# Optimization experiments

Measured on AMD Instinct MI355X. Metric: run time of the kernel, lower is better.

The kernel has to match this reference:

```python
import jax, jax.numpy as jnp
import numpy as np

B, S, D, H = 2, 2048, 1024, 16  # batch, seq, embed_dim, num_heads
DH = D // H                      # head dim = 64


def setup_inputs() -> dict:
    key = jax.random.key(0)
    kx, kq, kbq, kk, kbk, kv, kbv = jax.random.split(key, 7)
    scale = 1.0 / np.sqrt(D)
    return {
        "x": jax.random.normal(kx, (B, S, D), dtype=jnp.float32),
        "Wq": jax.random.normal(kq, (D, D), dtype=jnp.float32) * scale,
        "bq": jax.random.normal(kbq, (D,), dtype=jnp.float32) * 0.01,
        "Wk": jax.random.normal(kk, (D, D), dtype=jnp.float32) * scale,
        "bk": jax.random.normal(kbk, (D,), dtype=jnp.float32) * 0.01,
        "Wv": jax.random.normal(kv, (D, D), dtype=jnp.float32) * scale,
        "bv": jax.random.normal(kbv, (D,), dtype=jnp.float32) * 0.01,
    }


def reference(x, Wq, bq, Wk, bk, Wv, bv):
    # ooqkv_type == 'q', odeint_method == 'id': q branch = act(Linear(x)), exact GELU (torch nn.GELU default)
    q = jax.nn.gelu(x @ Wq + bq, approximate=False)
    k = x @ Wk + bk
    v = x @ Wv + bv
    # [B, S, D] -> [B, S, H, DH]
    q = q.reshape(B, S, H, DH)
    k = k.reshape(B, S, H, DH)
    v = v.reshape(B, S, H, DH)
    # NOTE: original module has NO 1/sqrt(d) scale — faithful reproduction
    att = jnp.einsum("bqhd,bkhd->bhqk", q, k)
    att = jax.nn.softmax(att, axis=-1)
    out = jnp.einsum("bhqk,bkhd->bqhd", att, v)
    return out.reshape(B, S, D)
```

## Files before the change

kernel.cpp:

```cpp
#include <hip/hip_runtime.h>
#include <math.h>

#define B_  2
#define S_  2048
#define D_  1024
#define H_  16
#define DH_ 64
#define M_  (B_ * S_)

typedef _Float16 half_t;
typedef __attribute__((ext_vector_type(8))) _Float16 h8;
typedef __attribute__((ext_vector_type(4))) _Float16 h4;
typedef __attribute__((ext_vector_type(4))) float   f32x4;

#define LOG2E 1.44269504088896f

__device__ __forceinline__ void gll16(const half_t* g, half_t* l) {
    __builtin_amdgcn_global_load_lds(
        (__attribute__((address_space(1))) const void*)g,
        (__attribute__((address_space(3))) void*)l, 16, 0, 0);
}

__global__ __launch_bounds__(256) void convert_x_k(
    const float* __restrict__ x, half_t* __restrict__ xh)
{
    const size_t i = ((size_t)blockIdx.x * 256 + threadIdx.x) * 8;
    const float4 a = *(const float4*)(x + i);
    const float4 b = *(const float4*)(x + i + 4);
    h8 o;
    o[0] = (half_t)a.x; o[1] = (half_t)a.y; o[2] = (half_t)a.z; o[3] = (half_t)a.w;
    o[4] = (half_t)b.x; o[5] = (half_t)b.y; o[6] = (half_t)b.z; o[7] = (half_t)b.w;
    *(h8*)(xh + i) = o;
}

__global__ __launch_bounds__(256) void transW_k(
    const float* __restrict__ Wq, const float* __restrict__ Wk,
    const float* __restrict__ Wv, half_t* __restrict__ Wt)
{
    const int which = blockIdx.y;
    const float* __restrict__ W = (which == 0) ? Wq : (which == 1) ? Wk : Wv;
    half_t* __restrict__ T = Wt + (size_t)which * D_ * D_;
    const int gw   = blockIdx.x * 4 + (threadIdx.x >> 6);
    const int lane = threadIdx.x & 63;
    const int n    = (gw & 15) * 64 + lane;
    const int k0   = (gw >> 4) * 8;
    h8 o;
    #pragma unroll
    for (int t = 0; t < 8; ++t) o[t] = (half_t)W[(size_t)(k0 + t) * D_ + n];
    *(h8*)(T + (size_t)n * D_ + k0) = o;
}

__global__ __launch_bounds__(256) void transV_k(
    const half_t* __restrict__ V, half_t* __restrict__ Vt)
{
    const int gw   = blockIdx.x * 4 + (threadIdx.x >> 6);
    const int lane = threadIdx.x & 63;
    const int bh   = gw >> 8;
    const int s0   = (gw & 255) * 8;
    const int b    = bh >> 4, h = bh & 15;
    h8 o;
    #pragma unroll
    for (int t = 0; t < 8; ++t)
        o[t] = V[((size_t)b * S_ + s0 + t) * D_ + h * DH_ + lane];
    *(h8*)(Vt + ((size_t)bh * DH_ + lane) * S_ + s0) = o;
}

__global__ __launch_bounds__(256) void qkv_gemm_f16(
    const half_t* __restrict__ xh, const half_t* __restrict__ Wt,
    const float* __restrict__ bq, const float* __restrict__ bk,
    const float* __restrict__ bv,
    half_t* __restrict__ Qo, half_t* __restrict__ Ko, half_t* __restrict__ Vo)
{
    const int n0g   = blockIdx.x * 128;
    const int which = n0g >> 10;
    const int n0    = n0g & 1023;
    const int m0    = blockIdx.y * 128;
    const half_t* __restrict__ Wp  = Wt + (size_t)which * D_ * D_;
    const float* __restrict__ bias = (which == 0) ? bq : (which == 1) ? bk : bv;
    half_t* __restrict__ out       = (which == 0) ? Qo : (which == 1) ? Ko : Vo;

    const int tid = threadIdx.x, lane = tid & 63, wave = tid >> 6;
    const int wm = (wave >> 1) * 64, wn = (wave & 1) * 64;
    const int ln = lane & 15, quad = lane >> 4;

    __shared__ __align__(16) half_t As[128][32];
    __shared__ __align__(16) half_t Bs[128][32];

    f32x4 acc[4][4];
    #pragma unroll
    for (int i = 0; i < 4; ++i)
        #pragma unroll
        for (int j = 0; j < 4; ++j) acc[i][j] = (f32x4){0.f, 0.f, 0.f, 0.f};

    for (int k0 = 0; k0 < D_; k0 += 32) {
        __syncthreads();
        #pragma unroll
        for (int l = 0; l < 2; ++l) {
            const int c = tid + l * 256;
            const int r = c >> 2, c8 = c & 3;
            gll16(xh + (size_t)(m0 + r) * D_ + k0 + c8 * 8, &As[r][c8 * 8]);
            gll16(Wp + (size_t)(n0 + r) * D_ + k0 + c8 * 8, &Bs[r][c8 * 8]);
        }
        __syncthreads();

        h8 af[4], bf[4];
        #pragma unroll
        for (int i = 0; i < 4; ++i) af[i] = *(const h8*)&As[wm + i * 16 + ln][quad * 8];
        #pragma unroll
        for (int j = 0; j < 4; ++j) bf[j] = *(const h8*)&Bs[wn + j * 16 + ln][quad * 8];
        #pragma unroll
        for (int i = 0; i < 4; ++i)
            #pragma unroll
            for (int j = 0; j < 4; ++j)
                acc[i][j] = __builtin_amdgcn_mfma_f32_16x16x32_f16(
                    af[i], bf[j], acc[i][j], 0, 0, 0);
    }

    #pragma unroll
    for (int j = 0; j < 4; ++j) {
        const int col = n0 + wn + j * 16 + ln;
        const float bb = bias[col];
        #pragma unroll
        for (int i = 0; i < 4; ++i) {
            #pragma unroll
            for (int r = 0; r < 4; ++r) {
                const int row = m0 + wm + i * 16 + quad * 4 + r;
                float t = acc[i][j][r] + bb;
                if (which == 0) {
                    const float u = t * fmaf(t * t, 0.0356774081f, 0.7978845608f);
                    const float e = __builtin_amdgcn_exp2f(u * -2.88539008178f);
                    t = t * __builtin_amdgcn_rcpf(1.0f + e) * LOG2E;
                }
                out[(size_t)row * D_ + col] = (half_t)t;
            }
        }
    }
}

__global__ __launch_bounds__(256) void attn_f16(
    const half_t* __restrict__ Q, const half_t* __restrict__ K,
    const half_t* __restrict__ Vt, float* __restrict__ out)
{
    const int tid  = threadIdx.x;
    const int lane = tid & 63;
    const int wave = tid >> 6;
    const int ln   = lane & 15;
    const int quad = lane >> 4;
    const int bh   = blockIdx.y;
    const int b    = bh >> 4;
    const int h    = bh & 15;
    const int q0   = blockIdx.x * 64;

    const half_t* __restrict__ Qb  = Q  + (size_t)b * S_ * D_ + h * DH_;
    const half_t* __restrict__ Kb  = K  + (size_t)b * S_ * D_ + h * DH_;
    const half_t* __restrict__ Vtb = Vt + (size_t)bh * DH_ * S_;

    __shared__ __align__(16) half_t Ks[64 * 64];
    __shared__ __align__(16) half_t Vs[64 * 64];
    __shared__ __align__(16) half_t QPs[64][72];

    #pragma unroll
    for (int l = 0; l < 2; ++l) {
        const int c = tid + l * 256;
        const int r = c >> 3, k8 = c & 7;
        *(h8*)&QPs[r][k8 * 8] = *(const h8*)(Qb + (size_t)(q0 + r) * D_ + k8 * 8);
    }
    __syncthreads();
    const h8 qb0 = *(const h8*)&QPs[wave * 16 + ln][quad * 8];
    const h8 qb1 = *(const h8*)&QPs[wave * 16 + ln][32 + quad * 8];

    h8 ones8;
    #pragma unroll
    for (int t = 0; t < 8; ++t) ones8[t] = (half_t)1.0f;

    f32x4 O[4];
    #pragma unroll
    for (int j = 0; j < 4; ++j) O[j] = (f32x4){0.f, 0.f, 0.f, 0.f};
    f32x4 l5 = (f32x4){0.f, 0.f, 0.f, 0.f};
    float m_i = -INFINITY;

    for (int k0 = 0; k0 < S_; k0 += 64) {
        __syncthreads();
        #pragma unroll
        for (int l = 0; l < 2; ++l) {
            const int c = tid + l * 256;
            const int r = c >> 3, c0 = c & 7;
            const int cs = c0 ^ (r & 7);
            gll16(Kb  + (size_t)(k0 + r) * D_ + cs * 8, &Ks[c * 8]);
            gll16(Vtb + (size_t)r * S_ + k0 + cs * 8,   &Vs[c * 8]);
        }
        __syncthreads();

        f32x4 s[4];
        #pragma unroll
        for (int j = 0; j < 4; ++j) {
            const int rK = j * 16 + ln;
            const h8 ka0 = *(const h8*)&Ks[rK * 64 + ((quad)     ^ (rK & 7)) * 8];
            const h8 ka1 = *(const h8*)&Ks[rK * 64 + ((quad + 4) ^ (rK & 7)) * 8];
            f32x4 t = (f32x4){0.f, 0.f, 0.f, 0.f};
            t = __builtin_amdgcn_mfma_f32_16x16x32_f16(ka0, qb0, t, 0, 0, 0);
            t = __builtin_amdgcn_mfma_f32_16x16x32_f16(ka1, qb1, t, 0, 0, 0);
            s[j] = t;
        }

        float mx = fmaxf(fmaxf(fmaxf(s[0][0], s[0][1]), fmaxf(s[0][2], s[0][3])),
                         fmaxf(fmaxf(s[1][0], s[1][1]), fmaxf(s[1][2], s[1][3])));
        mx = fmaxf(mx, fmaxf(fmaxf(fmaxf(s[2][0], s[2][1]), fmaxf(s[2][2], s[2][3])),
                             fmaxf(fmaxf(s[3][0], s[3][1]), fmaxf(s[3][2], s[3][3]))));
        mx = fmaxf(mx, __shfl_xor(mx, 16, 64));
        mx = fmaxf(mx, __shfl_xor(mx, 32, 64));

        if (__ballot(mx > m_i)) {
            const float mnew  = fmaxf(m_i, mx);
            const float alpha = __builtin_amdgcn_exp2f(m_i - mnew);
            m_i = mnew;
            float ar[4];
            #pragma unroll
            for (int r = 0; r < 4; ++r) ar[r] = __shfl(alpha, quad * 4 + r, 64);
            #pragma unroll
            for (int r = 0; r < 4; ++r) {
                l5[r] *= ar[r];
                #pragma unroll
                for (int j = 0; j < 4; ++j) O[j][r] *= ar[r];
            }
        }

        #pragma unroll
        for (int j = 0; j < 4; ++j) {
            h4 pv;
            #pragma unroll
            for (int r = 0; r < 4; ++r)
                pv[r] = (half_t)__builtin_amdgcn_exp2f(s[j][r] - m_i);
            *(h4*)&QPs[wave * 16 + ln][j * 16 + quad * 4] = pv;
        }

        const h8 pa0 = *(const h8*)&QPs[wave * 16 + ln][quad * 8];
        const h8 pa1 = *(const h8*)&QPs[wave * 16 + ln][32 + quad * 8];
        #pragma unroll
        for (int j = 0; j < 4; ++j) {
            const int rV = j * 16 + ln;
            const h8 vb0 = *(const h8*)&Vs[rV * 64 + ((quad)     ^ (rV & 7)) * 8];
            const h8 vb1 = *(const h8*)&Vs[rV * 64 + ((quad + 4) ^ (rV & 7)) * 8];
            O[j] = __builtin_amdgcn_mfma_f32_16x16x32_f16(pa0, vb0, O[j], 0, 0, 0);
            O[j] = __builtin_amdgcn_mfma_f32_16x16x32_f16(pa1, vb1, O[j], 0, 0, 0);
        }
        l5 = __builtin_amdgcn_mfma_f32_16x16x32_f16(pa0, ones8, l5, 0, 0, 0);
        l5 = __builtin_amdgcn_mfma_f32_16x16x32_f16(pa1, ones8, l5, 0, 0, 0);
    }

    #pragma unroll
    for (int r = 0; r < 4; ++r) {
        const float inv = 1.0f / l5[r];
        const int row = q0 + wave * 16 + quad * 4 + r;
        #pragma unroll
        for (int j = 0; j < 4; ++j)
            out[((size_t)b * S_ + row) * D_ + h * DH_ + j * 16 + ln] = O[j][r] * inv;
    }
}

extern "C" void kernel_launch(void* const* d_in, const int* in_sizes, int n_in,
                              void* d_out, int out_size, void* d_ws, size_t ws_size,
                              hipStream_t stream) {
    const float* x  = (const float*)d_in[0];
    const float* Wq = (const float*)d_in[1];
    const float* bq = (const float*)d_in[2];
    const float* Wk = (const float*)d_in[3];
    const float* bk = (const float*)d_in[4];
    const float* Wv = (const float*)d_in[5];
    const float* bv = (const float*)d_in[6];
    float* out = (float*)d_out;

    const size_t nmd = (size_t)M_ * D_;
    const size_t ndd = (size_t)D_ * D_;
    half_t* xh  = (half_t*)d_ws;
    half_t* Wt  = xh + nmd;
    half_t* Qh  = Wt + 3 * ndd;
    half_t* Kh  = Qh + nmd;
    half_t* Vh  = Kh + nmd;
    half_t* Vtw = Vh + nmd;

    convert_x_k<<<nmd / (256 * 8), 256, 0, stream>>>(x, xh);
    transW_k<<<dim3(512, 3), 256, 0, stream>>>(Wq, Wk, Wv, Wt);
    qkv_gemm_f16<<<dim3(3 * D_ / 128, M_ / 128), 256, 0, stream>>>(
        xh, Wt, bq, bk, bv, Qh, Kh, Vh);
    transV_k<<<2048, 256, 0, stream>>>(Vh, Vtw);
    attn_f16<<<dim3(S_ / 64, B_ * H_), 256, 0, stream>>>(Qh, Kh, Vtw, out);
}
```

Before: 197.9 us.

## Fuse prep kernels, write V transposed from GEMM, widen GEMM K-tile and attention Q-tile

```diff
diff --git a/kernel.cpp b/kernel.cpp
--- a/kernel.cpp
+++ b/kernel.cpp
@@ -21,55 +21,41 @@
         (__attribute__((address_space(3))) void*)l, 16, 0, 0);
 }
 
-__global__ __launch_bounds__(256) void convert_x_k(
-    const float* __restrict__ x, half_t* __restrict__ xh)
-{
-    const size_t i = ((size_t)blockIdx.x * 256 + threadIdx.x) * 8;
-    const float4 a = *(const float4*)(x + i);
-    const float4 b = *(const float4*)(x + i + 4);
-    h8 o;
-    o[0] = (half_t)a.x; o[1] = (half_t)a.y; o[2] = (half_t)a.z; o[3] = (half_t)a.w;
-    o[4] = (half_t)b.x; o[5] = (half_t)b.y; o[6] = (half_t)b.z; o[7] = (half_t)b.w;
-    *(h8*)(xh + i) = o;
-}
-
-__global__ __launch_bounds__(256) void transW_k(
+__global__ __launch_bounds__(256) void prep_k(
+    const float* __restrict__ x, half_t* __restrict__ xh,
     const float* __restrict__ Wq, const float* __restrict__ Wk,
     const float* __restrict__ Wv, half_t* __restrict__ Wt)
 {
-    const int which = blockIdx.y;
-    const float* __restrict__ W = (which == 0) ? Wq : (which == 1) ? Wk : Wv;
-    half_t* __restrict__ T = Wt + (size_t)which * D_ * D_;
-    const int gw   = blockIdx.x * 4 + (threadIdx.x >> 6);
-    const int lane = threadIdx.x & 63;
-    const int n    = (gw & 15) * 64 + lane;
-    const int k0   = (gw >> 4) * 8;
-    h8 o;
-    #pragma unroll
-    for (int t = 0; t < 8; ++t) o[t] = (half_t)W[(size_t)(k0 + t) * D_ + n];
-    *(h8*)(T + (size_t)n * D_ + k0) = o;
-}
-
-__global__ __launch_bounds__(256) void transV_k(
-    const half_t* __restrict__ V, half_t* __restrict__ Vt)
-{
-    const int gw   = blockIdx.x * 4 + (threadIdx.x >> 6);
-    const int lane = threadIdx.x & 63;
-    const int bh   = gw >> 8;
-    const int s0   = (gw & 255) * 8;
-    const int b    = bh >> 4, h = bh & 15;
-    h8 o;
-    #pragma unroll
-    for (int t = 0; t < 8; ++t)
-        o[t] = V[((size_t)b * S_ + s0 + t) * D_ + h * DH_ + lane];
-    *(h8*)(Vt + ((size_t)bh * DH_ + lane) * S_ + s0) = o;
+    const int bx = blockIdx.x;
+    if (bx < 2048) {
+        const size_t i = ((size_t)bx * 256 + threadIdx.x) * 8;
+        const float4 a = *(const float4*)(x + i);
+        const float4 b = *(const float4*)(x + i + 4);
+        h8 o;
+        o[0] = (half_t)a.x; o[1] = (half_t)a.y; o[2] = (half_t)a.z; o[3] = (half_t)a.w;
+        o[4] = (half_t)b.x; o[5] = (half_t)b.y; o[6] = (half_t)b.z; o[7] = (half_t)b.w;
+        *(h8*)(xh + i) = o;
+    } else {
+        const int gb    = bx - 2048;
+        const int which = gb >> 9;
+        const float* __restrict__ W = (which == 0) ? Wq : (which == 1) ? Wk : Wv;
+        half_t* __restrict__ T = Wt + (size_t)which * D_ * D_;
+        const int gw   = (gb & 511) * 4 + (threadIdx.x >> 6);
+        const int lane = threadIdx.x & 63;
+        const int n    = (gw & 15) * 64 + lane;
+        const int k0   = (gw >> 4) * 8;
+        h8 o;
+        #pragma unroll
+        for (int t = 0; t < 8; ++t) o[t] = (half_t)W[(size_t)(k0 + t) * D_ + n];
+        *(h8*)(T + (size_t)n * D_ + k0) = o;
+    }
 }
 
 __global__ __launch_bounds__(256) void qkv_gemm_f16(
     const half_t* __restrict__ xh, const half_t* __restrict__ Wt,
     const float* __restrict__ bq, const float* __restrict__ bk,
     const float* __restrict__ bv,
-    half_t* __restrict__ Qo, half_t* __restrict__ Ko, half_t* __restrict__ Vo)
+    half_t* __restrict__ Qo, half_t* __restrict__ Ko, half_t* __restrict__ Vt)
 {
     const int n0g   = blockIdx.x * 128;
     const int which = n0g >> 10;
@@ -77,14 +63,13 @@
     const int m0    = blockIdx.y * 128;
     const half_t* __restrict__ Wp  = Wt + (size_t)which * D_ * D_;
     const float* __restrict__ bias = (which == 0) ? bq : (which == 1) ? bk : bv;
-    half_t* __restrict__ out       = (which == 0) ? Qo : (which == 1) ? Ko : Vo;
 
     const int tid = threadIdx.x, lane = tid & 63, wave = tid >> 6;
     const int wm = (wave >> 1) * 64, wn = (wave & 1) * 64;
     const int ln = lane & 15, quad = lane >> 4;
 
-    __shared__ __align__(16) half_t As[128][32];
-    __shared__ __align__(16) half_t Bs[128][32];
+    __shared__ __align__(16) half_t As[128 * 64];
+    __shared__ __align__(16) half_t Bs[128 * 64];
 
     f32x4 acc[4][4];
     #pragma unroll
@@ -92,46 +77,75 @@
         #pragma unroll
         for (int j = 0; j < 4; ++j) acc[i][j] = (f32x4){0.f, 0.f, 0.f, 0.f};
 
-    for (int k0 = 0; k0 < D_; k0 += 32) {
+    for (int k0 = 0; k0 < D_; k0 += 64) {
         __syncthreads();
         #pragma unroll
-        for (int l = 0; l < 2; ++l) {
-            const int c = tid + l * 256;
-            const int r = c >> 2, c8 = c & 3;
-            gll16(xh + (size_t)(m0 + r) * D_ + k0 + c8 * 8, &As[r][c8 * 8]);
-            gll16(Wp + (size_t)(n0 + r) * D_ + k0 + c8 * 8, &Bs[r][c8 * 8]);
+        for (int l = 0; l < 4; ++l) {
+            const int c  = tid + l * 256;
+            const int r  = c >> 3, c0 = c & 7;
+            const int cs = c0 ^ (r & 7);
+            gll16(xh + (size_t)(m0 + r) * D_ + k0 + cs * 8, &As[c * 8]);
+            gll16(Wp + (size_t)(n0 + r) * D_ + k0 + cs * 8, &Bs[c * 8]);
         }
         __syncthreads();
 
-        h8 af[4], bf[4];
-        #pragma unroll
-        for (int i = 0; i < 4; ++i) af[i] = *(const h8*)&As[wm + i * 16 + ln][quad * 8];
-        #pragma unroll
-        for (int j = 0; j < 4; ++j) bf[j] = *(const h8*)&Bs[wn + j * 16 + ln][quad * 8];
-        #pragma unroll
-        for (int i = 0; i < 4; ++i)
-            #pragma unroll
-            for (int j = 0; j < 4; ++j)
-                acc[i][j] = __builtin_amdgcn_mfma_f32_16x16x32_f16(
-                    af[i], bf[j], acc[i][j], 0, 0, 0);
-    }
-
-    #pragma unroll
-    for (int j = 0; j < 4; ++j) {
-        const int col = n0 + wn + j * 16 + ln;
-        const float bb = bias[col];
-        #pragma unroll
-        for (int i = 0; i < 4; ++i) {
-            #pragma unroll
-            for (int r = 0; r < 4; ++r) {
-                const int row = m0 + wm + i * 16 + quad * 4 + r;
-                float t = acc[i][j][r] + bb;
-                if (which == 0) {
-                    const float u = t * fmaf(t * t, 0.0356774081f, 0.7978845608f);
-                    const float e = __builtin_amdgcn_exp2f(u * -2.88539008178f);
-                    t = t * __builtin_amdgcn_rcpf(1.0f + e) * LOG2E;
+        #pragma unroll
+        for (int kc = 0; kc < 2; ++kc) {
+            h8 af[4], bf[4];
+            #pragma unroll
+            for (int i = 0; i < 4; ++i) {
+                const int r = wm + i * 16 + ln;
+                af[i] = *(const h8*)&As[r * 64 + (((kc << 2) + quad) ^ (r & 7)) * 8];
+            }
+            #pragma unroll
+            for (int j = 0; j < 4; ++j) {
+                const int r = wn + j * 16 + ln;
+                bf[j] = *(const h8*)&Bs[r * 64 + (((kc << 2) + quad) ^ (r & 7)) * 8];
+            }
+            #pragma unroll
+            for (int i = 0; i < 4; ++i)
+                #pragma unroll
+                for (int j = 0; j < 4; ++j)
+                    acc[i][j] = __builtin_amdgcn_mfma_f32_16x16x32_f16(
+                        af[i], bf[j], acc[i][j], 0, 0, 0);
+        }
+    }
+
+    if (which == 2) {
+        #pragma unroll
+        for (int j = 0; j < 4; ++j) {
+            const int col = n0 + wn + j * 16 + ln;
+            const int h = col >> 6, d = col & 63;
+            const float bb = bias[col];
+            #pragma unroll
+            for (int i = 0; i < 4; ++i) {
+                const int sg = m0 + wm + i * 16 + quad * 4;
+                const int b  = sg >> 11, srow = sg & 2047;
+                h4 pv;
+                #pragma unroll
+                for (int r = 0; r < 4; ++r) pv[r] = (half_t)(acc[i][j][r] + bb);
+                *(h4*)(Vt + (((size_t)(b * H_ + h) * DH_ + d) * S_ + srow)) = pv;
+            }
+        }
+    } else {
+        half_t* __restrict__ out = (which == 0) ? Qo : Ko;
+        #pragma unroll
+        for (int j = 0; j < 4; ++j) {
+            const int col = n0 + wn + j * 16 + ln;
+            const float bb = bias[col];
+            #pragma unroll
+            for (int i = 0; i < 4; ++i) {
+                #pragma unroll
+                for (int r = 0; r < 4; ++r) {
+                    const int row = m0 + wm + i * 16 + quad * 4 + r;
+                    float t = acc[i][j][r] + bb;
+                    if (which == 0) {
+                        const float u = t * fmaf(t * t, 0.0356774081f, 0.7978845608f);
+                        const float e = __builtin_amdgcn_exp2f(u * -2.88539008178f);
+                        t = t * __builtin_amdgcn_rcpf(1.0f + e) * LOG2E;
+                    }
+                    out[(size_t)row * D_ + col] = (half_t)t;
                 }
-                out[(size_t)row * D_ + col] = (half_t)t;
             }
         }
     }
@@ -149,7 +163,7 @@
     const int bh   = blockIdx.y;
     const int b    = bh >> 4;
     const int h    = bh & 15;
-    const int q0   = blockIdx.x * 64;
+    const int q0   = blockIdx.x * 128;
 
     const half_t* __restrict__ Qb  = Q  + (size_t)b * S_ * D_ + h * DH_;
     const half_t* __restrict__ Kb  = K  + (size_t)b * S_ * D_ + h * DH_;
@@ -157,104 +171,138 @@
 
     __shared__ __align__(16) half_t Ks[64 * 64];
     __shared__ __align__(16) half_t Vs[64 * 64];
-    __shared__ __align__(16) half_t QPs[64][72];
-
-    #pragma unroll
-    for (int l = 0; l < 2; ++l) {
+    __shared__ __align__(16) half_t QPs[128][72];
+
+    #pragma unroll
+    for (int l = 0; l < 4; ++l) {
         const int c = tid + l * 256;
         const int r = c >> 3, k8 = c & 7;
         *(h8*)&QPs[r][k8 * 8] = *(const h8*)(Qb + (size_t)(q0 + r) * D_ + k8 * 8);
     }
     __syncthreads();
-    const h8 qb0 = *(const h8*)&QPs[wave * 16 + ln][quad * 8];
-    const h8 qb1 = *(const h8*)&QPs[wave * 16 + ln][32 + quad * 8];
+    const h8 qa0 = *(const h8*)&QPs[wave * 32 + ln][quad * 8];
+    const h8 qa1 = *(const h8*)&QPs[wave * 32 + ln][32 + quad * 8];
+    const h8 qc0 = *(const h8*)&QPs[wave * 32 + 16 + ln][quad * 8];
+    const h8 qc1 = *(const h8*)&QPs[wave * 32 + 16 + ln][32 + quad * 8];
 
     h8 ones8;
     #pragma unroll
     for (int t = 0; t < 8; ++t) ones8[t] = (half_t)1.0f;
 
-    f32x4 O[4];
-    #pragma unroll
-    for (int j = 0; j < 4; ++j) O[j] = (f32x4){0.f, 0.f, 0.f, 0.f};
-    f32x4 l5 = (f32x4){0.f, 0.f, 0.f, 0.f};
-    float m_i = -INFINITY;
+    f32x4 Oa[4], Ob[4];
+    #pragma unroll
+    for (int j = 0; j < 4; ++j) {
+        Oa[j] = (f32x4){0.f, 0.f, 0.f, 0.f};
+        Ob[j] = (f32x4){0.f, 0.f, 0.f, 0.f};
+    }
+    f32x4 la = (f32x4){0.f, 0.f, 0.f, 0.f};
+    f32x4 lb = (f32x4){0.f, 0.f, 0.f, 0.f};
+    float m_a = -INFINITY, m_b = -INFINITY;
 
     for (int k0 = 0; k0 < S_; k0 += 64) {
         __syncthreads();
         #pragma unroll
         for (int l = 0; l < 2; ++l) {
-            const int c = tid + l * 256;
-            const int r = c >> 3, c0 = c & 7;
+            const int c  = tid + l * 256;
+            const int r  = c >> 3, c0 = c & 7;
             const int cs = c0 ^ (r & 7);
             gll16(Kb  + (size_t)(k0 + r) * D_ + cs * 8, &Ks[c * 8]);
             gll16(Vtb + (size_t)r * S_ + k0 + cs * 8,   &Vs[c * 8]);
         }
         __syncthreads();
 
-        f32x4 s[4];
+        f32x4 sa[4], sb[4];
         #pragma unroll
         for (int j = 0; j < 4; ++j) {
             const int rK = j * 16 + ln;
             const h8 ka0 = *(const h8*)&Ks[rK * 64 + ((quad)     ^ (rK & 7)) * 8];
             const h8 ka1 = *(const h8*)&Ks[rK * 64 + ((quad + 4) ^ (rK & 7)) * 8];
             f32x4 t = (f32x4){0.f, 0.f, 0.f, 0.f};
-            t = __builtin_amdgcn_mfma_f32_16x16x32_f16(ka0, qb0, t, 0, 0, 0);
-            t = __builtin_amdgcn_mfma_f32_16x16x32_f16(ka1, qb1, t, 0, 0, 0);
-            s[j] = t;
-        }
-
-        float mx = fmaxf(fmaxf(fmaxf(s[0][0], s[0][1]), fmaxf(s[0][2], s[0][3])),
-                         fmaxf(fmaxf(s[1][0], s[1][1]), fmaxf(s[1][2], s[1][3])));
-        mx = fmaxf(mx, fmaxf(fmaxf(fmaxf(s[2][0], s[2][1]), fmaxf(s[2][2], s[2][3])),
-                             fmaxf(fmaxf(s[3][0], s[3][1]), fmaxf(s[3][2], s[3][3]))));
-        mx = fmaxf(mx, __shfl_xor(mx, 16, 64));
-        mx = fmaxf(mx, __shfl_xor(mx, 32, 64));
-
-        if (__ballot(mx > m_i)) {
-            const float mnew  = fmaxf(m_i, mx);
-            const float alpha = __builtin_amdgcn_exp2f(m_i - mnew);
-            m_i = mnew;
-            float ar[4];
-            #pragma unroll
-            for (int r = 0; r < 4; ++r) ar[r] = __shfl(alpha, quad * 4 + r, 64);
+            t = __builtin_amdgcn_mfma_f32_16x16x32_f16(ka0, qa0, t, 0, 0, 0);
+            t = __builtin_amdgcn_mfma_f32_16x16x32_f16(ka1, qa1, t, 0, 0, 0);
+            sa[j] = t;
+            f32x4 u = (f32x4){0.f, 0.f, 0.f, 0.f};
+            u = __builtin_amdgcn_mfma_f32_16x16x32_f16(ka0, qc0, u, 0, 0, 0);
+            u = __builtin_amdgcn_mfma_f32_16x16x32_f16(ka1, qc1, u, 0, 0, 0);
+            sb[j] = u;
+        }
+
+        float mxa = sa[0][0], mxb = sb[0][0];
+        #pragma unroll
+        for (int j = 0; j < 4; ++j)
             #pragma unroll
             for (int r = 0; r < 4; ++r) {
-                l5[r] *= ar[r];
+                mxa = fmaxf(mxa, sa[j][r]);
+                mxb = fmaxf(mxb, sb[j][r]);
+            }
+        mxa = fmaxf(mxa, __shfl_xor(mxa, 16, 64));
+        mxa = fmaxf(mxa, __shfl_xor(mxa, 32, 64));
+        mxb = fmaxf(mxb, __shfl_xor(mxb, 16, 64));
+        mxb = fmaxf(mxb, __shfl_xor(mxb, 32, 64));
+
+        if (__ballot(mxa > m_a || mxb > m_b)) {
+            const float mna = fmaxf(m_a, mxa);
+            const float mnb = fmaxf(m_b, mxb);
+            const float ala = __builtin_amdgcn_exp2f(m_a - mna);
+            const float alb = __builtin_amdgcn_exp2f(m_b - mnb);
+            m_a = mna; m_b = mnb;
+            float ra[4], rb[4];
+            #pragma unroll
+            for (int r = 0; r < 4; ++r) {
+                ra[r] = __shfl(ala, quad * 4 + r, 64);
+                rb[r] = __shfl(alb, quad * 4 + r, 64);
+            }
+            #pragma unroll
+            for (int r = 0; r < 4; ++r) {
+                la[r] *= ra[r]; lb[r] *= rb[r];
                 #pragma unroll
-                for (int j = 0; j < 4; ++j) O[j][r] *= ar[r];
-            }
-        }
-
-        #pragma unroll
-        for (int j = 0; j < 4; ++j) {
-            h4 pv;
-            #pragma unroll
-            for (int r = 0; r < 4; ++r)
-                pv[r] = (half_t)__builtin_amdgcn_exp2f(s[j][r] - m_i);
-            *(h4*)&QPs[wave * 16 + ln][j * 16 + quad * 4] = pv;
-        }
-
-        const h8 pa0 = *(const h8*)&QPs[wave * 16 + ln][quad * 8];
-        const h8 pa1 = *(const h8*)&QPs[wave * 16 + ln][32 + quad * 8];
+                for (int j = 0; j < 4; ++j) { Oa[j][r] *= ra[r]; Ob[j][r] *= rb[r]; }
+            }
+        }
+
+        #pragma unroll
+        for (int j = 0; j < 4; ++j) {
+            h4 pva, pvb;
+            #pragma unroll
+            for (int r = 0; r < 4; ++r) {
+                pva[r] = (half_t)__builtin_amdgcn_exp2f(sa[j][r] - m_a);
+                pvb[r] = (half_t)__builtin_amdgcn_exp2f(sb[j][r] - m_b);
+            }
+            *(h4*)&QPs[wave * 32 + ln][j * 16 + quad * 4]      = pva;
+            *(h4*)&QPs[wave * 32 + 16 + ln][j * 16 + quad * 4] = pvb;
+        }
+
+        const h8 pa0 = *(const h8*)&QPs[wave * 32 + ln][quad * 8];
+        const h8 pa1 = *(const h8*)&QPs[wave * 32 + ln][32 + quad * 8];
+        const h8 pb0 = *(const h8*)&QPs[wave * 32 + 16 + ln][quad * 8];
+        const h8 pb1 = *(const h8*)&QPs[wave * 32 + 16 + ln][32 + quad * 8];
         #pragma unroll
         for (int j = 0; j < 4; ++j) {
             const int rV = j * 16 + ln;
             const h8 vb0 = *(const h8*)&Vs[rV * 64 + ((quad)     ^ (rV & 7)) * 8];
             const h8 vb1 = *(const h8*)&Vs[rV * 64 + ((quad + 4) ^ (rV & 7)) * 8];
-            O[j] = __builtin_amdgcn_mfma_f32_16x16x32_f16(pa0, vb0, O[j], 0, 0, 0);
-            O[j] = __builtin_amdgcn_mfma_f32_16x16x32_f16(pa1, vb1, O[j], 0, 0, 0);
-        }
-        l5 = __builtin_amdgcn_mfma_f32_16x16x32_f16(pa0, ones8, l5, 0, 0, 0);
-        l5 = __builtin_amdgcn_mfma_f32_16x16x32_f16(pa1, ones8, l5, 0, 0, 0);
+            Oa[j] = __builtin_amdgcn_mfma_f32_16x16x32_f16(pa0, vb0, Oa[j], 0, 0, 0);
+            Oa[j] = __builtin_amdgcn_mfma_f32_16x16x32_f16(pa1, vb1, Oa[j], 0, 0, 0);
+            Ob[j] = __builtin_amdgcn_mfma_f32_16x16x32_f16(pb0, vb0, Ob[j], 0, 0, 0);
+            Ob[j] = __builtin_amdgcn_mfma_f32_16x16x32_f16(pb1, vb1, Ob[j], 0, 0, 0);
+        }
+        la = __builtin_amdgcn_mfma_f32_16x16x32_f16(pa0, ones8, la, 0, 0, 0);
+        la = __builtin_amdgcn_mfma_f32_16x16x32_f16(pa1, ones8, la, 0, 0, 0);
+        lb = __builtin_amdgcn_mfma_f32_16x16x32_f16(pb0, ones8, lb, 0, 0, 0);
+        lb = __builtin_amdgcn_mfma_f32_16x16x32_f16(pb1, ones8, lb, 0, 0, 0);
     }
 
     #pragma unroll
     for (int r = 0; r < 4; ++r) {
-        const float inv = 1.0f / l5[r];
-        const int row = q0 + wave * 16 + quad * 4 + r;
-        #pragma unroll
-        for (int j = 0; j < 4; ++j)
-            out[((size_t)b * S_ + row) * D_ + h * DH_ + j * 16 + ln] = O[j][r] * inv;
+        const float iva = 1.0f / la[r];
+        const float ivb = 1.0f / lb[r];
+        const int rowa = q0 + wave * 32 + quad * 4 + r;
+        const int rowb = rowa + 16;
+        #pragma unroll
+        for (int j = 0; j < 4; ++j) {
+            out[((size_t)b * S_ + rowa) * D_ + h * DH_ + j * 16 + ln] = Oa[j][r] * iva;
+            out[((size_t)b * S_ + rowb) * D_ + h * DH_ + j * 16 + ln] = Ob[j][r] * ivb;
+        }
     }
 }
 
@@ -276,13 +324,10 @@
     half_t* Wt  = xh + nmd;
     half_t* Qh  = Wt + 3 * ndd;
     half_t* Kh  = Qh + nmd;
-    half_t* Vh  = Kh + nmd;
-    half_t* Vtw = Vh + nmd;
-
-    convert_x_k<<<nmd / (256 * 8), 256, 0, stream>>>(x, xh);
-    transW_k<<<dim3(512, 3), 256, 0, stream>>>(Wq, Wk, Wv, Wt);
+    half_t* Vtw = Kh + nmd;
+
+    prep_k<<<2048 + 1536, 256, 0, stream>>>(x, xh, Wq, Wk, Wv, Wt);
     qkv_gemm_f16<<<dim3(3 * D_ / 128, M_ / 128), 256, 0, stream>>>(
-        xh, Wt, bq, bk, bv, Qh, Kh, Vh);
-    transV_k<<<2048, 256, 0, stream>>>(Vh, Vtw);
-    attn_f16<<<dim3(S_ / 64, B_ * H_), 256, 0, stream>>>(Qh, Kh, Vtw, out);
-}
+        xh, Wt, bq, bk, bv, Qh, Kh, Vtw);
+    attn_f16<<<dim3(S_ / 128, B_ * H_), 256, 0, stream>>>(Qh, Kh, Vtw, out);
+}
```

After: 196.0 us. No clear change (-1.0%).
